# Kernel optimization log

Measured on AMD Instinct MI355X. Metric: run time of the kernel, lower is better.

The kernel has to match this reference:

```python
import jax, jax.numpy as jnp
import numpy as np

NUM_Q_HEADS = 32
NUM_KV_HEADS = 8
GROUP = NUM_Q_HEADS // NUM_KV_HEADS  # 4, matches hardcoded repeat_interleave(repeats=4)
HEAD_DIM = 128
ROPE_BASE = 10000.0


def _rope_cos_sin(seq_len, head_dim, dtype):
    # [S, D/2] angle tables for rotate-half RoPE
    inv_freq = 1.0 / (ROPE_BASE ** (jnp.arange(0, head_dim, 2, dtype=jnp.float32) / head_dim))
    ang = jnp.arange(seq_len, dtype=jnp.float32)[:, None] * inv_freq[None, :]
    return jnp.cos(ang).astype(dtype), jnp.sin(ang).astype(dtype)


def _apply_rope(x, cos, sin):
    # x: [B, S, H, D]; cos/sin: [S, D/2] broadcast over batch & heads
    x1, x2 = jnp.split(x, 2, axis=-1)
    c = cos[None, :, None, :]
    s = sin[None, :, None, :]
    return jnp.concatenate([x1 * c - x2 * s, x2 * c + x1 * s], axis=-1)


def setup_inputs() -> dict:
    key = jax.random.key(0)
    k1, k2, k3 = jax.random.split(key, 3)
    B, S, E = 2, 2048, 4096
    x = jax.random.normal(k1, (B, S, E), dtype=jnp.float32)
    w_in = jax.random.normal(k2, (6144, E), dtype=jnp.float32) * 0.02   # torch Linear weight [out, in]
    w_out = jax.random.normal(k3, (E, E), dtype=jnp.float32) * 0.02
    return {"x": x, "w_in": w_in, "w_out": w_out}


def reference(x, w_in, w_out):
    B, S, E = x.shape
    D = HEAD_DIM
    qkv = jnp.einsum('bse,fe->bsf', x, w_in)  # [B, S, 6144]
    parts = jnp.split(qkv, GROUP + 2, axis=-1)  # 6 equal chunks of width E//GROUP
    q = jnp.concatenate(parts[:GROUP], axis=-1).reshape(B, S, NUM_Q_HEADS, D)
    k = parts[GROUP].reshape(B, S, NUM_KV_HEADS, D)
    v = parts[GROUP + 1].reshape(B, S, NUM_KV_HEADS, D)

    cos, sin = _rope_cos_sin(S, D, x.dtype)
    q = _apply_rope(q, cos, sin)
    k = _apply_rope(k, cos, sin)

    # GQA without materializing repeated K/V: group q heads by kv head.
    # repeat_interleave(k, 4, dim=2) maps q head h -> kv head h // 4, i.e. q view [B,S,HKV,G,D]
    qg = q.reshape(B, S, NUM_KV_HEADS, GROUP, D)
    scale = 1.0 / jnp.sqrt(jnp.asarray(D, dtype=x.dtype))
    scores = jnp.einsum('bqhgd,bkhd->bhgqk', qg, k) * scale  # [B, HKV, G, S, S]
    causal = jnp.tril(jnp.ones((S, S), dtype=bool))
    scores = jnp.where(causal[None, None, None, :, :], scores, jnp.asarray(-1e30, dtype=scores.dtype))
    probs = jax.nn.softmax(scores, axis=-1)
    out = jnp.einsum('bhgqk,bkhd->bqhgd', probs, v)  # [B, S, HKV, G, D]
    out = out.reshape(B, S, E)
    return jnp.einsum('bse,fe->bsf', out, w_out)
```

## Files before the change

### kernel.cpp

```cpp
#include <hip/hip_runtime.h>
#include <hip/hip_bf16.h>
#include <stdint.h>

typedef unsigned short u16;
typedef __bf16 bf16x8 __attribute__((ext_vector_type(8)));
typedef u16 u16x8 __attribute__((ext_vector_type(8)));
typedef float f32x4 __attribute__((ext_vector_type(4)));
typedef float f32x16 __attribute__((ext_vector_type(16)));
typedef uint32_t u32x4 __attribute__((ext_vector_type(4)));

#define DEV __device__ __forceinline__
#define SBAR() asm volatile("s_barrier" ::: "memory")
#define SCHEDB() __builtin_amdgcn_sched_barrier(0)
#define LGKM0() do { asm volatile("s_waitcnt lgkmcnt(0)" ::: "memory"); SCHEDB(); } while (0)

DEV u16 f2bf(float f) {
  uint32_t u = __builtin_bit_cast(uint32_t, f);
  return (u16)((u + 0x7FFFu + ((u >> 16) & 1u)) >> 16);
}
DEV float bf2f(u16 h) { return __builtin_bit_cast(float, (uint32_t)h << 16); }

DEV void gload_lds16(const void* g, void* l) {
  __builtin_amdgcn_global_load_lds((const __attribute__((address_space(1))) uint32_t*)g,
                                   (__attribute__((address_space(3))) uint32_t*)l, 16, 0, 0);
}

DEV uint32_t cvtpk(float lo, float hi) {
  uint32_t r;
  asm("v_cvt_pk_bf16_f32 %0, %1, %2" : "=v"(r) : "v"(lo), "v"(hi));
  return r;
}
DEV void plswap(uint32_t& a, uint32_t& b) {
  asm("v_permlane32_swap_b32 %0, %1" : "+v"(a), "+v"(b));
}

__global__ void cvt_bf16(const float* __restrict__ in, u16* __restrict__ out, int n) {
  int i = (blockIdx.x * 256 + threadIdx.x) * 8;
  if (i >= n) return;
  const float4* p = reinterpret_cast<const float4*>(in + i);
  float4 a = p[0], b = p[1];
  u16x8 o;
  o[0] = f2bf(a.x); o[1] = f2bf(a.y); o[2] = f2bf(a.z); o[3] = f2bf(a.w);
  o[4] = f2bf(b.x); o[5] = f2bf(b.y); o[6] = f2bf(b.z); o[7] = f2bf(b.w);
  *reinterpret_cast<u16x8*>(out + i) = o;
}

__global__ void rope_table(float* __restrict__ ct, float* __restrict__ st) {
  int i = blockIdx.x * 256 + threadIdx.x;
  int s = i >> 6, d = i & 63;
  float invf = powf(10000.0f, -(float)d * (1.0f / 64.0f));
  float ang = (float)s * invf;
  ct[i] = cosf(ang);
  st[i] = sinf(ang);
}

__global__ void rope_apply(u16* __restrict__ qkv, const float* __restrict__ ct, const float* __restrict__ st) {
  int idx = blockIdx.x * 256 + threadIdx.x;
  int grp = idx & 7;
  int head = (idx >> 3) % 40;
  int row = idx / 320;
  int s = row & 2047;
  size_t f0 = head < 32 ? (size_t)head * 128 : (size_t)4096 + (size_t)(head - 32) * 128;
  u16* p = qkv + (size_t)row * 6144 + f0 + grp * 8;
  u16x8 a = *reinterpret_cast<const u16x8*>(p);
  u16x8 b = *reinterpret_cast<const u16x8*>(p + 64);
  const float4* cp = reinterpret_cast<const float4*>(ct + s * 64 + grp * 8);
  const float4* sp = reinterpret_cast<const float4*>(st + s * 64 + grp * 8);
  float4 c0 = cp[0], c1 = cp[1], s0 = sp[0], s1 = sp[1];
  float cc[8] = {c0.x, c0.y, c0.z, c0.w, c1.x, c1.y, c1.z, c1.w};
  float ss[8] = {s0.x, s0.y, s0.z, s0.w, s1.x, s1.y, s1.z, s1.w};
  u16x8 o1, o2;
#pragma unroll
  for (int i = 0; i < 8; i++) {
    float x1 = bf2f(a[i]), x2 = bf2f(b[i]);
    o1[i] = f2bf(x1 * cc[i] - x2 * ss[i]);
    o2[i] = f2bf(x2 * cc[i] + x1 * ss[i]);
  }
  *reinterpret_cast<u16x8*>(p) = o1;
  *reinterpret_cast<u16x8*>(p + 64) = o2;
}

__global__ void prep_vt(const u16* __restrict__ qkv, u16* __restrict__ vtg) {
  int id = blockIdx.x;
  int j = id & 31, kvh = (id >> 5) & 7, b = id >> 8;
  const int tid = threadIdx.x;
  const size_t rowB = (size_t)b * 2048;
  u16* img = vtg + (size_t)id * 8192;
#pragma unroll
  for (int p = 0; p < 4; p++) {
    int lin = p * 256 + tid;
    int d = lin >> 3, c = lin & 7;
    const u16* src = qkv + (rowB + j * 64 + c * 8) * 6144 + 5120 + kvh * 128 + d;
    u16x8 v;
#pragma unroll
    for (int i = 0; i < 8; i++) v[i] = src[(size_t)i * 6144];
    *reinterpret_cast<u16x8*>(img + d * 64 + ((c ^ (d & 7)) << 3)) = v;
  }
}

DEV void store_c(float* C, size_t idx, float v) { C[idx] = v; }
DEV void store_c(u16* C, size_t idx, float v) { C[idx] = f2bf(v); }

template <typename OutT>
__global__ __launch_bounds__(512, 2) void gemm256(const u16* __restrict__ A, const u16* __restrict__ B,
                                                  OutT* __restrict__ C, int M, int N, int K, int ldc) {
  __shared__ __align__(16) u16 lds[65536];
  char* LB = (char*)lds;
  const int tid = threadIdx.x;
  const int w = tid >> 6, lane = tid & 63;
  const int l15 = lane & 15, l4 = lane >> 4;
  const int wm = w >> 2, wn = w & 3;

  int nwg = gridDim.x;
  int q = nwg >> 3, rr = nwg & 7;
  int xcd = blockIdx.x & 7, idx = blockIdx.x >> 3;
  int sw = (xcd < rr ? xcd * (q + 1) : rr * (q + 1) + (xcd - rr) * q) + idx;
  int gxn = N >> 8;
  int by = sw / gxn, bx = sw - by * gxn;
  const int row0 = by << 8, col0 = bx << 8;
  const int NT = K >> 6;

  const int srow = w * 8 + (lane >> 3);
  const int sc16 = (lane & 7) ^ ((lane >> 3) & 7);
  const u16* gA = A + (size_t)(row0 + srow) * K + sc16 * 8;
  const u16* gB = B + (size_t)(col0 + srow) * K + sc16 * 8;

  const int fl = (l15 & 7) << 4;
  const int aoff = (wm * 128 + l15) * 128 + l4 * 16;
  const int boff = (wn * 64 + l15) * 128 + l4 * 16;

  f32x4 acc[8][4] = {};
  bf16x8 fA[4][2], fB0[2][2], fBc[2][2];

#define STAGE_A(kt, h, base)                                                      \
  {                                                                               \
    const u16* g_ = gA + (size_t)((h)*128) * K + (size_t)(kt)*64;                 \
    gload_lds16(g_, (base) + (h)*16384 + w * 1024);                               \
    gload_lds16(g_ + (size_t)64 * K, (base) + (h)*16384 + 8192 + w * 1024);       \
  }
#define STAGE_B(kt, h, base)                                                      \
  {                                                                               \
    const u16* g_ = gB + (size_t)((h)*128) * K + (size_t)(kt)*64;                 \
    gload_lds16(g_, (base) + (h)*16384 + w * 1024);                               \
    gload_lds16(g_ + (size_t)64 * K, (base) + (h)*16384 + 8192 + w * 1024);       \
  }
#define MFMA_Q(FB, MH, NH)                                                        \
  _Pragma("unroll") for (int kk = 0; kk < 2; kk++) {                              \
    _Pragma("unroll") for (int mf = 0; mf < 4; mf++) {                            \
      _Pragma("unroll") for (int nf = 0; nf < 2; nf++) {                          \
        acc[(MH)*4 + mf][(NH)*2 + nf] = __builtin_amdgcn_mfma_f32_16x16x32_bf16(  \
            fA[mf][kk], FB[nf][kk], acc[(MH)*4 + mf][(NH)*2 + nf], 0, 0, 0);      \
      }                                                                           \
    }                                                                             \
  }

  STAGE_A(0, 0, LB);
  STAGE_A(0, 1, LB);
  STAGE_B(0, 0, LB + 65536);
  STAGE_B(0, 1, LB + 65536);
  STAGE_A(1, 0, LB + 32768);
  STAGE_B(1, 0, LB + 98304);
  STAGE_B(1, 1, LB + 98304);
  asm volatile("s_waitcnt vmcnt(6)" ::: "memory");
  SBAR();

  for (int t = 0; t < NT; ++t) {
    char* ac = LB + (t & 1) * 32768;
    char* bc = LB + 65536 + (t & 1) * 32768;
    char* an = LB + ((t + 1) & 1) * 32768;

#pragma unroll
    for (int mf = 0; mf < 4; mf++)
#pragma unroll
      for (int kk = 0; kk < 2; kk++)
        fA[mf][kk] = *(const bf16x8*)(ac + ((aoff + mf * 2048 + kk * 64) ^ fl));
#pragma unroll
    for (int nf = 0; nf < 2; nf++)
#pragma unroll
      for (int kk = 0; kk < 2; kk++)
        fB0[nf][kk] = *(const bf16x8*)(bc + ((boff + nf * 2048 + kk * 64) ^ fl));
    if (t + 1 < NT) STAGE_A(t + 1, 1, an);
    SBAR();
    LGKM0();
    __builtin_amdgcn_s_setprio(1);
    MFMA_Q(fB0, 0, 0);
    __builtin_amdgcn_s_setprio(0);
    SBAR();

#pragma unroll
    for (int nf = 0; nf < 2; nf++)
#pragma unroll
      for (int kk = 0; kk < 2; kk++)
        fBc[nf][kk] = *(const bf16x8*)(bc + ((boff + (nf + 2) * 2048 + kk * 64) ^ fl));
    SBAR();
    LGKM0();
    __builtin_amdgcn_s_setprio(1);
    MFMA_Q(fBc, 0, 1);
    __builtin_amdgcn_s_setprio(0);
    SBAR();

#pragma unroll
    for (int mf = 0; mf < 4; mf++)
#pragma unroll
      for (int kk = 0; kk < 2; kk++)
        fA[mf][kk] = *(const bf16x8*)(ac + ((aoff + (mf + 4) * 2048 + kk * 64) ^ fl));
    if (t + 2 < NT) {
      STAGE_B(t + 2, 0, bc);
      STAGE_B(t + 2, 1, bc);
    }
    SBAR();
    LGKM0();
    __builtin_amdgcn_s_setprio(1);
    MFMA_Q(fBc, 1, 1);
    __builtin_amdgcn_s_setprio(0);
    SBAR();

    if (t + 2 < NT) STAGE_A(t + 2, 0, ac);
    __builtin_amdgcn_s_setprio(1);
    MFMA_Q(fB0, 1, 0);
    __builtin_amdgcn_s_setprio(0);
    if (t + 2 < NT) {
      asm volatile("s_waitcnt vmcnt(6)" ::: "memory");
      SBAR();
    } else if (t + 1 < NT) {
      asm volatile("s_waitcnt vmcnt(0)" ::: "memory");
      SBAR();
    }
  }

#pragma unroll
  for (int mf = 0; mf < 8; mf++)
#pragma unroll
    for (int nf = 0; nf < 4; nf++)
#pragma unroll
      for (int r = 0; r < 4; r++) {
        size_t row = (size_t)row0 + wm * 128 + mf * 16 + l4 * 4 + r;
        size_t col = (size_t)col0 + wn * 64 + nf * 16 + l15;
        store_c(C, row * (size_t)ldc + col, acc[mf][nf][r]);
      }
#undef STAGE_A
#undef STAGE_B
#undef MFMA_Q
}

__global__ __launch_bounds__(512, 2) void gemm_bn128(const u16* __restrict__ A, const u16* __restrict__ B,
                                                     u16* __restrict__ C, int M, int N, int K, int ldc) {
  __shared__ __align__(16) u16 lds[49152];
  char* LB = (char*)lds;
  const int tid = threadIdx.x;
  const int w = tid >> 6, lane = tid & 63;
  const int l15 = lane & 15, l4 = lane >> 4;
  const int wm = w >> 2, wn = w & 3;

  int nwg = gridDim.x;
  int q = nwg >> 3, rr = nwg & 7;
  int xcd = blockIdx.x & 7, idx = blockIdx.x >> 3;
  int sw = (xcd < rr ? xcd * (q + 1) : rr * (q + 1) + (xcd - rr) * q) + idx;
  int gxn = N >> 7;
  int by = sw / gxn, bx = sw - by * gxn;
  const int row0 = by << 8, col0 = bx << 7;
  const int NT = K >> 6;

  const int srow = w * 8 + (lane >> 3);
  const int sc16 = (lane & 7) ^ ((lane >> 3) & 7);
  const u16* gA = A + (size_t)(row0 + srow) * K + sc16 * 8;
  const u16* gB = B + (size_t)(col0 + srow) * K + sc16 * 8;

  const int fl = (l15 & 7) << 4;
  const int aoff = (wm * 128 + l15) * 128 + l4 * 16;
  const int boff = (wn * 32 + l15) * 128 + l4 * 16;

  f32x4 acc[8][2] = {};
  bf16x8 fA[4][2], fB[2][2];

#define STAGE_A(kt, h, base)                                                      \
  {                                                                               \
    const u16* g_ = gA + (size_t)((h)*128) * K + (size_t)(kt)*64;                 \
    gload_lds16(g_, (base) + (h)*16384 + w * 1024);                               \
    gload_lds16(g_ + (size_t)64 * K, (base) + (h)*16384 + 8192 + w * 1024);       \
  }
#define STAGE_B(kt, base)                                                         \
  {                                                                               \
    const u16* g_ = gB + (size_t)(kt)*64;                                         \
    gload_lds16(g_, (base) + w * 1024);                                           \
    gload_lds16(g_ + (size_t)64 * K, (base) + 8192 + w * 1024);                   \
  }

  STAGE_A(0, 0, LB);
  STAGE_A(0, 1, LB);
  STAGE_B(0, LB + 65536);
  STAGE_A(1, 0, LB + 32768);
  STAGE_B(1, LB + 65536 + 16384);
  asm volatile("s_waitcnt vmcnt(4)" ::: "memory");
  SBAR();

  for (int t = 0; t < NT; ++t) {
    char* ac = LB + (t & 1) * 32768;
    char* bc = LB + 65536 + (t & 1) * 16384;
    char* an = LB + ((t + 1) & 1) * 32768;

#pragma unroll
    for (int mf = 0; mf < 4; mf++)
#pragma unroll
      for (int kk = 0; kk < 2; kk++)
        fA[mf][kk] = *(const bf16x8*)(ac + ((aoff + mf * 2048 + kk * 64) ^ fl));
#pragma unroll
    for (int nf = 0; nf < 2; nf++)
#pragma unroll
      for (int kk = 0; kk < 2; kk++)
        fB[nf][kk] = *(const bf16x8*)(bc + ((boff + nf * 2048 + kk * 64) ^ fl));
    if (t + 1 < NT) STAGE_A(t + 1, 1, an);
    SBAR();
    LGKM0();
    __builtin_amdgcn_s_setprio(1);
#pragma unroll
    for (int kk = 0; kk < 2; kk++)
#pragma unroll
      for (int mf = 0; mf < 4; mf++)
#pragma unroll
        for (int nf = 0; nf < 2; nf++)
          acc[mf][nf] = __builtin_amdgcn_mfma_f32_16x16x32_bf16(fA[mf][kk], fB[nf][kk], acc[mf][nf], 0, 0, 0);
    __builtin_amdgcn_s_setprio(0);
    SBAR();

#pragma unroll
    for (int mf = 0; mf < 4; mf++)
#pragma unroll
      for (int kk = 0; kk < 2; kk++)
        fA[mf][kk] = *(const bf16x8*)(ac + ((aoff + (mf + 4) * 2048 + kk * 64) ^ fl));
    if (t + 2 < NT) STAGE_B(t + 2, bc);
    SBAR();
    LGKM0();
    __builtin_amdgcn_s_setprio(1);
#pragma unroll
    for (int kk = 0; kk < 2; kk++)
#pragma unroll
      for (int mf = 0; mf < 4; mf++)
#pragma unroll
        for (int nf = 0; nf < 2; nf++)
          acc[mf + 4][nf] = __builtin_amdgcn_mfma_f32_16x16x32_bf16(fA[mf][kk], fB[nf][kk], acc[mf + 4][nf], 0, 0, 0);
    __builtin_amdgcn_s_setprio(0);
    SBAR();

    if (t + 2 < NT) {
      STAGE_A(t + 2, 0, ac);
      asm volatile("s_waitcnt vmcnt(4)" ::: "memory");
      SBAR();
    } else if (t + 1 < NT) {
      asm volatile("s_waitcnt vmcnt(0)" ::: "memory");
      SBAR();
    }
  }

#pragma unroll
  for (int mf = 0; mf < 8; mf++)
#pragma unroll
    for (int nf = 0; nf < 2; nf++)
#pragma unroll
      for (int r = 0; r < 4; r++) {
        size_t row = (size_t)row0 + wm * 128 + mf * 16 + l4 * 4 + r;
        size_t col = (size_t)col0 + wn * 32 + nf * 16 + l15;
        C[row * (size_t)ldc + col] = f2bf(acc[mf][nf][r]);
      }
#undef STAGE_A
#undef STAGE_B
}

__global__ __launch_bounds__(256, 2) void attn_fwd(const u16* __restrict__ qkv,
                                                   const u16* __restrict__ vtg,
                                                   u16* __restrict__ out) {
  constexpr int S = 2048, F = 6144, E = 4096;
  __shared__ __align__(16) u16 Kt[2 * 8192];
  __shared__ __align__(16) u16 Vt[2 * 8192];

  const int tid = threadIdx.x;
  const int w = tid >> 6, lane = tid & 63;
  const int l31 = lane & 31, hi = lane >> 5;
  const int pair = blockIdx.x;
  const int b = blockIdx.y >> 5, h = blockIdx.y & 31, kvh = h >> 2;
  const size_t rowB = (size_t)b * S;
  const float sc = 0.08838834764831845f * 1.4426950408889634f;
  const int sgn = tid >> 4, sgc = tid & 15;
  const size_t vtb = (size_t)(b * 8 + kvh) * 32 * 8192;

  auto stage = [&](int j, int buf) {
    char* kd = ((char*)Kt) + buf * 16384 + w * 1024;
    char* vd = ((char*)Vt) + buf * 16384 + w * 1024;
    const u16* vs = vtg + vtb + (size_t)j * 8192 + tid * 8;
#pragma unroll
    for (int p = 0; p < 4; p++) {
      int n = p * 16 + sgn;
      const u16* g = qkv + (rowB + j * 64 + n) * F + 4096 + kvh * 128 + (sgc ^ (n & 7)) * 8;
      gload_lds16(g, kd + p * 4096);
      gload_lds16(vs + p * 2048, vd + p * 4096);
    }
  };

  for (int half = 0; half < 2; ++half) {
    const int t = half ? 15 - pair : pair;
    const int nt = 2 * t + 2;
    const int r0 = t * 128;
    const int qg = r0 + w * 32 + l31;

    bf16x8 qf[8];
    {
      const u16* qp = qkv + (rowB + qg) * F + h * 128 + hi * 8;
#pragma unroll
      for (int ds = 0; ds < 8; ds++) qf[ds] = *reinterpret_cast<const bf16x8*>(qp + ds * 16);
    }

    f32x16 acco[4] = {};
    float m = -1e30f, l = 0.f;

    stage(0, 0);
    __syncthreads();

    for (int j = 0; j < nt; ++j) {
      const int cur = j & 1;
      if (j + 1 < nt) stage(j + 1, cur ^ 1);

      const char* kbase = ((const char*)Kt) + cur * 16384;
      f32x16 s0 = {}, s1 = {};
      __builtin_amdgcn_s_setprio(1);
#pragma unroll
      for (int ds = 0; ds < 8; ds++) {
        int ch = ((2 * ds + hi) ^ (l31 & 7)) << 4;
        bf16x8 k0 = *reinterpret_cast<const bf16x8*>(kbase + l31 * 256 + ch);
        bf16x8 k1 = *reinterpret_cast<const bf16x8*>(kbase + (32 + l31) * 256 + ch);
        s0 = __builtin_amdgcn_mfma_f32_32x32x16_bf16(k0, qf[ds], s0, 0, 0, 0);
        s1 = __builtin_amdgcn_mfma_f32_32x32x16_bf16(k1, qf[ds], s1, 0, 0, 0);
      }
      __builtin_amdgcn_s_setprio(0);

      f32x16 px0, px1;
      if (j >= 2 * t) {
#pragma unroll
        for (int rg = 0; rg < 16; rg++) {
          int kv0 = j * 64 + (rg & 3) + 8 * (rg >> 2) + 4 * hi;
          px0[rg] = (kv0 > qg) ? -1e30f : s0[rg] * sc;
          px1[rg] = (kv0 + 32 > qg) ? -1e30f : s1[rg] * sc;
        }
      } else {
#pragma unroll
        for (int rg = 0; rg < 16; rg++) {
          px0[rg] = s0[rg] * sc;
          px1[rg] = s1[rg] * sc;
        }
      }

      float mt[8];
#pragma unroll
      for (int i = 0; i < 8; i++)
        mt[i] = fmaxf(fmaxf(px0[i], px0[i + 8]), fmaxf(px1[i], px1[i + 8]));
#pragma unroll
      for (int stp = 4; stp; stp >>= 1)
#pragma unroll
        for (int i = 0; i < stp; i++) mt[i] = fmaxf(mt[i], mt[i + stp]);
      float pm = fmaxf(mt[0], __shfl_xor(mt[0], 32));

      if (__any(pm > m + 8.0f)) {
        float mn = fmaxf(m, pm);
        float fr = exp2f(m - mn);
        m = mn;
        l *= fr;
#pragma unroll
        for (int rg = 0; rg < 16; rg++) {
          int qrow = (rg & 3) + 8 * (rg >> 2) + 4 * hi;
          float frq = __builtin_bit_cast(
              float, __builtin_amdgcn_ds_bpermute(qrow << 2, __builtin_bit_cast(int, fr)));
          acco[0][rg] *= frq;
          acco[1][rg] *= frq;
          acco[2][rg] *= frq;
          acco[3][rg] *= frq;
        }
      }

#pragma unroll
      for (int rg = 0; rg < 16; rg++) {
        px0[rg] = exp2f(px0[rg] - m);
        px1[rg] = exp2f(px1[rg] - m);
      }
      float at[8];
#pragma unroll
      for (int i = 0; i < 8; i++)
        at[i] = (px0[i] + px0[i + 8]) + (px1[i] + px1[i + 8]);
#pragma unroll
      for (int stp = 4; stp; stp >>= 1)
#pragma unroll
        for (int i = 0; i < stp; i++) at[i] += at[i + stp];
      l += at[0] + __shfl_xor(at[0], 32);

      const char* vbase = ((const char*)Vt) + cur * 16384;
      __builtin_amdgcn_s_setprio(1);
#define PV_STEP(PH, SS)                                                               \
  {                                                                                   \
    uint32_t X0 = cvtpk(PH[((SS)&1) * 8 + 0], PH[((SS)&1) * 8 + 1]);                  \
    uint32_t Y0 = cvtpk(PH[((SS)&1) * 8 + 4], PH[((SS)&1) * 8 + 5]);                  \
    uint32_t X1 = cvtpk(PH[((SS)&1) * 8 + 2], PH[((SS)&1) * 8 + 3]);                  \
    uint32_t Y1 = cvtpk(PH[((SS)&1) * 8 + 6], PH[((SS)&1) * 8 + 7]);                  \
    plswap(X0, Y0);                                                                   \
    plswap(X1, Y1);                                                                   \
    u32x4 pw = {X0, X1, Y0, Y1};                                                      \
    bf16x8 pa = __builtin_bit_cast(bf16x8, pw);                                       \
    _Pragma("unroll") for (int df = 0; df < 4; df++) {                                \
      bf16x8 vf = *reinterpret_cast<const bf16x8*>(                                   \
          vbase + (32 * df + l31) * 128 + (((2 * (SS) + hi) ^ (l31 & 7)) << 4));      \
      acco[df] = __builtin_amdgcn_mfma_f32_32x32x16_bf16(pa, vf, acco[df], 0, 0, 0);  \
    }                                                                                 \
  }
      PV_STEP(px0, 0)
      PV_STEP(px0, 1)
      PV_STEP(px1, 2)
      PV_STEP(px1, 3)
#undef PV_STEP
      __builtin_amdgcn_s_setprio(0);

      __syncthreads();
    }

    float linv = 1.f / l;
#pragma unroll
    for (int rg = 0; rg < 16; rg++) {
      int qrow = (rg & 3) + 8 * (rg >> 2) + 4 * hi;
      float lv = __builtin_bit_cast(
          float, __builtin_amdgcn_ds_bpermute(qrow << 2, __builtin_bit_cast(int, linv)));
      size_t row = rowB + r0 + w * 32 + qrow;
      u16* op = out + row * E + h * 128 + l31;
#pragma unroll
      for (int df = 0; df < 4; df++) op[df * 32] = f2bf(acco[df][rg] * lv);
    }
  }
}

extern "C" void kernel_launch(void* const* d_in, const int* in_sizes, int n_in,
                              void* d_out, int out_size, void* d_ws, size_t ws_size,
                              hipStream_t stream) {
  const float* x = (const float*)d_in[0];
  const float* w_in = (const float*)d_in[1];
  const float* w_out = (const float*)d_in[2];
  float* out = (float*)d_out;
  char* ws = (char*)d_ws;

  u16* xb = (u16*)(ws);
  u16* wib = (u16*)(ws + 33554432ull);
  u16* wob = (u16*)(ws + 83886080ull);
  u16* qkvb = (u16*)(ws + 117440512ull);
  float* ct = (float*)(ws + 167772160ull);
  float* st = ct + 2048 * 64;
  u16* attnb = xb;
  u16* vtg = wib;

  cvt_bf16<<<8192, 256, 0, stream>>>(x, xb, 16777216);
  cvt_bf16<<<12288, 256, 0, stream>>>(w_in, wib, 25165824);
  cvt_bf16<<<8192, 256, 0, stream>>>(w_out, wob, 16777216);
  rope_table<<<512, 256, 0, stream>>>(ct, st);
  gemm256<u16><<<256, 512, 0, stream>>>(xb, wib, qkvb, 4096, 4096, 4096, 6144);
  gemm_bn128<<<256, 512, 0, stream>>>(xb, wib + (size_t)4096 * 4096, qkvb + 4096, 4096, 2048, 4096, 6144);
  rope_apply<<<5120, 256, 0, stream>>>(qkvb, ct, st);
  prep_vt<<<512, 256, 0, stream>>>(qkvb, vtg);
  attn_fwd<<<dim3(8, 64), 256, 0, stream>>>(qkvb, vtg, attnb);
  gemm256<float><<<256, 512, 0, stream>>>(attnb, wob, out, 4096, 4096, 4096, 4096);
}
```

Measured before the change: 510.1 us.

## Restructure 256x256 GEMM main loop with register double-buffered fragments and unroll-by-two

```diff
diff --git a/kernel.cpp b/kernel.cpp
--- a/kernel.cpp
+++ b/kernel.cpp
@@ -130,7 +130,7 @@
   const int boff = (wn * 64 + l15) * 128 + l4 * 16;
 
   f32x4 acc[8][4] = {};
-  bf16x8 fA[4][2], fB0[2][2], fBc[2][2];
+  bf16x8 fAL[4][2], fAH[4][2], fB1[2][2], fB0e[2][2], fB0o[2][2];
 
 #define STAGE_A(kt, h, base)                                                      \
   {                                                                               \
@@ -144,12 +144,24 @@
     gload_lds16(g_, (base) + (h)*16384 + w * 1024);                               \
     gload_lds16(g_ + (size_t)64 * K, (base) + (h)*16384 + 8192 + w * 1024);       \
   }
-#define MFMA_Q(FB, MH, NH)                                                        \
+#define READ_AL(base)                                                             \
+  _Pragma("unroll") for (int mf = 0; mf < 4; mf++)                                \
+    _Pragma("unroll") for (int kk = 0; kk < 2; kk++)                              \
+      fAL[mf][kk] = *(const bf16x8*)((base) + ((aoff + mf * 2048 + kk * 64) ^ fl));
+#define READ_AH(base)                                                             \
+  _Pragma("unroll") for (int mf = 0; mf < 4; mf++)                                \
+    _Pragma("unroll") for (int kk = 0; kk < 2; kk++)                              \
+      fAH[mf][kk] = *(const bf16x8*)((base) + ((aoff + (mf + 4) * 2048 + kk * 64) ^ fl));
+#define READ_B(FB, base, nh)                                                      \
+  _Pragma("unroll") for (int nf = 0; nf < 2; nf++)                                \
+    _Pragma("unroll") for (int kk = 0; kk < 2; kk++)                              \
+      FB[nf][kk] = *(const bf16x8*)((base) + ((boff + (nf + 2 * (nh)) * 2048 + kk * 64) ^ fl));
+#define MFMA_Q(FA, FB, MH, NH)                                                    \
   _Pragma("unroll") for (int kk = 0; kk < 2; kk++) {                              \
     _Pragma("unroll") for (int mf = 0; mf < 4; mf++) {                            \
       _Pragma("unroll") for (int nf = 0; nf < 2; nf++) {                          \
         acc[(MH)*4 + mf][(NH)*2 + nf] = __builtin_amdgcn_mfma_f32_16x16x32_bf16(  \
-            fA[mf][kk], FB[nf][kk], acc[(MH)*4 + mf][(NH)*2 + nf], 0, 0, 0);      \
+            FA[mf][kk], FB[nf][kk], acc[(MH)*4 + mf][(NH)*2 + nf], 0, 0, 0);      \
       }                                                                           \
     }                                                                             \
   }
@@ -158,74 +170,65 @@
   STAGE_A(0, 1, LB);
   STAGE_B(0, 0, LB + 65536);
   STAGE_B(0, 1, LB + 65536);
-  STAGE_A(1, 0, LB + 32768);
   STAGE_B(1, 0, LB + 98304);
   STAGE_B(1, 1, LB + 98304);
-  asm volatile("s_waitcnt vmcnt(6)" ::: "memory");
+  STAGE_A(1, 0, LB + 32768);
+  STAGE_A(1, 1, LB + 32768);
+  asm volatile("s_waitcnt vmcnt(8)" ::: "memory");
   SBAR();
-
-  for (int t = 0; t < NT; ++t) {
-    char* ac = LB + (t & 1) * 32768;
-    char* bc = LB + 65536 + (t & 1) * 32768;
-    char* an = LB + ((t + 1) & 1) * 32768;
-
-#pragma unroll
-    for (int mf = 0; mf < 4; mf++)
-#pragma unroll
-      for (int kk = 0; kk < 2; kk++)
-        fA[mf][kk] = *(const bf16x8*)(ac + ((aoff + mf * 2048 + kk * 64) ^ fl));
-#pragma unroll
-    for (int nf = 0; nf < 2; nf++)
-#pragma unroll
-      for (int kk = 0; kk < 2; kk++)
-        fB0[nf][kk] = *(const bf16x8*)(bc + ((boff + nf * 2048 + kk * 64) ^ fl));
-    if (t + 1 < NT) STAGE_A(t + 1, 1, an);
-    SBAR();
-    LGKM0();
-    __builtin_amdgcn_s_setprio(1);
-    MFMA_Q(fB0, 0, 0);
-    __builtin_amdgcn_s_setprio(0);
-    SBAR();
-
-#pragma unroll
-    for (int nf = 0; nf < 2; nf++)
-#pragma unroll
-      for (int kk = 0; kk < 2; kk++)
-        fBc[nf][kk] = *(const bf16x8*)(bc + ((boff + (nf + 2) * 2048 + kk * 64) ^ fl));
-    SBAR();
-    LGKM0();
-    __builtin_amdgcn_s_setprio(1);
-    MFMA_Q(fBc, 0, 1);
-    __builtin_amdgcn_s_setprio(0);
-    SBAR();
-
-#pragma unroll
-    for (int mf = 0; mf < 4; mf++)
-#pragma unroll
-      for (int kk = 0; kk < 2; kk++)
-        fA[mf][kk] = *(const bf16x8*)(ac + ((aoff + (mf + 4) * 2048 + kk * 64) ^ fl));
-    if (t + 2 < NT) {
-      STAGE_B(t + 2, 0, bc);
-      STAGE_B(t + 2, 1, bc);
-    }
-    SBAR();
-    LGKM0();
-    __builtin_amdgcn_s_setprio(1);
-    MFMA_Q(fBc, 1, 1);
-    __builtin_amdgcn_s_setprio(0);
-    SBAR();
-
-    if (t + 2 < NT) STAGE_A(t + 2, 0, ac);
-    __builtin_amdgcn_s_setprio(1);
-    MFMA_Q(fB0, 1, 0);
-    __builtin_amdgcn_s_setprio(0);
-    if (t + 2 < NT) {
-      asm volatile("s_waitcnt vmcnt(6)" ::: "memory");
-      SBAR();
-    } else if (t + 1 < NT) {
-      asm volatile("s_waitcnt vmcnt(0)" ::: "memory");
-      SBAR();
-    }
+  READ_AL(LB);
+  READ_B(fB0e, LB + 65536, 0);
+  SCHEDB();
+
+#define TILE_BODY(t, AC, BC, AN, BN, FB0C, FB0N)                                  \
+  {                                                                               \
+                                                                          \
+    LGKM0();                                                                      \
+    READ_B(fB1, BC, 1);                                                           \
+    SCHEDB();                                                                     \
+    __builtin_amdgcn_s_setprio(1);                                                \
+    MFMA_Q(fAL, FB0C, 0, 0);                                                      \
+    __builtin_amdgcn_s_setprio(0);                                                \
+    SBAR();                                                                       \
+                                                                          \
+    if ((t) + 2 < NT) STAGE_B((t) + 2, 0, BC);                                    \
+    LGKM0();                                                                      \
+    READ_AH(AC);                                                                  \
+    SCHEDB();                                                                     \
+    __builtin_amdgcn_s_setprio(1);                                                \
+    MFMA_Q(fAL, fB1, 0, 1);                                                       \
+    __builtin_amdgcn_s_setprio(0);                                                \
+    SBAR();                                                                       \
+                                                                          \
+    if ((t) + 2 < NT) STAGE_B((t) + 2, 1, BC);                                    \
+    LGKM0();                                                                      \
+    __builtin_amdgcn_s_setprio(1);                                                \
+    MFMA_Q(fAH, fB1, 1, 1);                                                       \
+    __builtin_amdgcn_s_setprio(0);                                                \
+    if ((t) + 2 < NT) {                                                           \
+      asm volatile("s_waitcnt vmcnt(4)" ::: "memory");                            \
+    } else if ((t) + 1 < NT) {                                                    \
+      asm volatile("s_waitcnt vmcnt(0)" ::: "memory");                            \
+    }                                                                             \
+    SBAR();                                                                       \
+                                                                          \
+    if ((t) + 2 < NT) {                                                           \
+      STAGE_A((t) + 2, 0, AC);                                                    \
+      STAGE_A((t) + 2, 1, AC);                                                    \
+    }                                                                             \
+    if ((t) + 1 < NT) {                                                           \
+      READ_AL(AN);                                                                \
+      READ_B(FB0N, BN, 0);                                                        \
+    }                                                                             \
+    SCHEDB();                                                                     \
+    __builtin_amdgcn_s_setprio(1);                                                \
+    MFMA_Q(fAH, FB0C, 1, 0);                                                      \
+    __builtin_amdgcn_s_setprio(0);                                                \
+  }
+
+  for (int t = 0; t < NT; t += 2) {
+    TILE_BODY(t, LB, LB + 65536, LB + 32768, LB + 98304, fB0e, fB0o);
+    TILE_BODY(t + 1, LB + 32768, LB + 98304, LB, LB + 65536, fB0o, fB0e);
   }
 
 #pragma unroll
@@ -240,7 +243,11 @@
       }
 #undef STAGE_A
 #undef STAGE_B
+#undef READ_AL
+#undef READ_AH
+#undef READ_B
 #undef MFMA_Q
+#undef TILE_BODY
 }
 
 __global__ __launch_bounds__(512, 2) void gemm_bn128(const u16* __restrict__ A, const u16* __restrict__ B,
```

Result: slower. 1.751 ms (+243.2%).
